# Kernel tuning notes

Hardware: AMD Instinct MI355X
Metric: run time of the kernel (lower is better)

Reference implementation:

```python
import jax, jax.numpy as jnp
import numpy as np

N = 100000
INC = 128
GRID = 256
S = 2  # scale s for voxel_to_aux coarse pooling


def _ln(x, g, b, eps=1e-6):
    m = jnp.mean(x, axis=-1, keepdims=True)
    v = jnp.var(x, axis=-1, keepdims=True)
    return (x - m) / jnp.sqrt(v + eps) * g + b


def setup_inputs() -> dict:
    rng = np.random.default_rng(0)
    lin = rng.choice(GRID ** 3, size=N, replace=False)
    x = (lin // (GRID * GRID)).astype(np.int64)
    y = ((lin // GRID) % GRID).astype(np.int64)
    z = (lin % GRID).astype(np.int64)
    coords = np.stack([x, y, z], axis=1).astype(np.int32)
    # sparse 3x3x3 neighbor table (pad index = N for missing neighbors)
    order = np.argsort(lin)
    lin_sorted = lin[order]
    nbr_idx = np.full((N, 27), N, dtype=np.int32)
    k = 0
    for dx in (-1, 0, 1):
        for dy in (-1, 0, 1):
            for dz in (-1, 0, 1):
                nx, ny, nz = x + dx, y + dy, z + dz
                valid = (nx >= 0) & (nx < GRID) & (ny >= 0) & (ny < GRID) & (nz >= 0) & (nz < GRID)
                nlin = (nx * GRID + ny) * GRID + nz
                pos = np.clip(np.searchsorted(lin_sorted, nlin), 0, N - 1)
                found = valid & (lin_sorted[pos] == nlin)
                nbr_idx[:, k] = np.where(found, order[pos].astype(np.int32), N)
                k += 1
    # voxel_to_aux: coarse voxel id at scale S; counts per coarse voxel
    G2 = GRID // S
    clin = ((x // S) * G2 + (y // S)) * G2 + (z // S)
    uniq, aux_idx, counts = np.unique(clin, return_inverse=True, return_counts=True)
    counts_v = counts[aux_idx].astype(np.float32)
    num_aux = int(len(uniq))

    key = jax.random.key(0)
    ks = jax.random.split(key, 6)
    sd = 1.0 / np.sqrt(INC)
    return {
        "F": jax.random.normal(ks[0], (N, INC), jnp.float32),
        "coords": jnp.asarray(coords),
        "nbr_idx": jnp.asarray(nbr_idx),
        "aux_idx": jnp.asarray(aux_idx.astype(np.int32)),
        "counts_v": jnp.asarray(counts_v),
        "num_aux": num_aux,
        "alpha": jnp.ones((1, INC), jnp.float32),
        "w_pos": jax.random.normal(ks[1], (INC, 3), jnp.float32) * (1.0 / np.sqrt(3.0)),
        "w_pre": jax.random.normal(ks[2], (INC, INC), jnp.float32) * sd,
        "g_pre": jnp.ones((INC,), jnp.float32),
        "b_pre": jnp.zeros((INC,), jnp.float32),
        "w_conv": jax.random.normal(ks[3], (27, INC, INC), jnp.float32) * (sd / np.sqrt(27.0)),
        "g_local": jnp.ones((INC,), jnp.float32),
        "b_local": jnp.zeros((INC,), jnp.float32),
        "g_norm": jnp.ones((INC,), jnp.float32),
        "b_norm": jnp.zeros((INC,), jnp.float32),
    }


def reference(F, coords, nbr_idx, aux_idx, counts_v, num_aux, alpha, w_pos, w_pre,
              g_pre, b_pre, w_conv, g_local, b_local, g_norm, b_norm):
    inc = F.shape[1]
    # pre_mix: Linear (no bias) + LayerNorm
    F_input = _ln(F @ w_pre.T, g_pre, b_pre)
    # local_mix: sparse 3x3x3 conv on ORIGINAL features via neighbor gather
    Fp = jnp.concatenate([F, jnp.zeros((1, inc), F.dtype)], axis=0)
    gathered = Fp[nbr_idx]                               # [N, 27, inc]
    local = jnp.einsum('nkc,kcd->nd', gathered, w_conv)  # [N, inc]
    # cos_x positional reweighting
    pos = (coords.astype(jnp.float32) @ w_pos.T) * alpha  # [N, inc]
    psin, pcos = jnp.sin(pos), jnp.cos(pos)
    cat = jnp.concatenate([F_input * pcos, F_input * psin, F_input * pos], axis=1)  # [N, 3*inc]
    # voxel_to_aux (sum pool per coarse voxel) + aux_to_voxel (mean broadcast back)
    aux = jax.ops.segment_sum(cat, aux_idx, num_segments=num_aux)
    vox = aux[aux_idx] / counts_v[:, None]
    new = (vox[:, :inc] * pcos + vox[:, inc:2 * inc] * psin
           + (vox[:, 2 * inc:] - F_input * pos))
    new = _ln(new, g_norm, b_norm)
    local = _ln(local, g_local, b_local)
    return jax.nn.relu(new + local)
```

## Files before the change

kernel.cpp:

```cpp
#include <hip/hip_runtime.h>
#include <hip/hip_bf16.h>
#include <stdint.h>

#define N_PTS 100000
#define INC 128
#define NSLOT 27
#define CAPP 8192
#define SCAP 64

typedef float f32x4 __attribute__((ext_vector_type(4)));
typedef short bf16x8 __attribute__((ext_vector_type(8)));

static const size_t OFF_WP   = 0;
static const size_t SZ_WP    = (size_t)NSLOT * INC * INC * 2;
static const size_t OFF_WPRE = (OFF_WP + SZ_WP + 255) & ~(size_t)255;
static const size_t SZ_WPRE  = (size_t)INC * INC * 2;
static const size_t OFF_FIN  = (OFF_WPRE + SZ_WPRE + 255) & ~(size_t)255;
static const size_t SZ_FIN   = (size_t)N_PTS * INC * 2;
static const size_t OFF_LOC  = (OFF_FIN + SZ_FIN + 255) & ~(size_t)255;
static const size_t SZ_LOC   = (size_t)N_PTS * INC * 4;
static const size_t OFF_LOC2 = (OFF_LOC + SZ_LOC + 255) & ~(size_t)255;
static const size_t SZ_LOC2  = (size_t)N_PTS * INC * 4;
static const size_t OFF_CNT  = (OFF_LOC2 + SZ_LOC2 + 255) & ~(size_t)255;
static const size_t SZ_CNT   = 128;
static const size_t OFF_DST  = (OFF_CNT + SZ_CNT + 255) & ~(size_t)255;
static const size_t SZ_DST   = (size_t)26 * CAPP * 4;
static const size_t OFF_SRC  = (OFF_DST + SZ_DST + 255) & ~(size_t)255;
static const size_t SZ_SRC   = (size_t)26 * CAPP * 4;
static const size_t OFF_FLG  = (OFF_SRC + SZ_SRC + 255) & ~(size_t)255;
static const size_t SZ_FLG   = (size_t)N_PTS;
static const size_t OFF_NDL  = (OFF_FLG + SZ_FLG + 255) & ~(size_t)255;
static const size_t SZ_NDL   = (size_t)N_PTS * 4;

#define PREP_BLOCKS 1792
#define SCAN_BLOCKS 391
#define MT64 1563
#define PAIRB 256

__device__ __forceinline__ float compute_pos3(float w0, float w1, float w2, float a,
                                              float cx, float cy, float cz) {
    return (cx * w0 + cy * w1 + cz * w2) * a;
}

__device__ __forceinline__ bf16x8 ld_cvt8(const float* __restrict__ p) {
    const float4 u = *(const float4*)p;
    const float4 v = *(const float4*)(p + 4);
    bf16x8 r;
    __hip_bfloat16* h = (__hip_bfloat16*)&r;
    h[0] = __float2bfloat16(u.x); h[1] = __float2bfloat16(u.y);
    h[2] = __float2bfloat16(u.z); h[3] = __float2bfloat16(u.w);
    h[4] = __float2bfloat16(v.x); h[5] = __float2bfloat16(v.y);
    h[6] = __float2bfloat16(v.z); h[7] = __float2bfloat16(v.w);
    return r;
}

__global__ __launch_bounds__(256) void k_front(
        const float* __restrict__ w_pre, const float* __restrict__ w_conv,
        __hip_bfloat16* __restrict__ Wp, __hip_bfloat16* __restrict__ Wpre,
        const int* __restrict__ nbr_idx, const float* __restrict__ counts_v,
        int* __restrict__ cnt, int* __restrict__ dst, int* __restrict__ src,
        unsigned char* __restrict__ flg, int* __restrict__ ndl,
        float* __restrict__ loc2) {
    __shared__ int s_cnt[26], s_base[26];
    __shared__ int s_dst[26][SCAP], s_src[26][SCAP];

    const int tid = threadIdx.x;

    if (blockIdx.x < PREP_BLOCKS) {
        int i = blockIdx.x * 256 + tid;
        if (i < 16384) {
            int d = i >> 7, c = i & 127;
            int j = ((c >> 5) << 12) | ((d >> 4) << 9)
                  | (((((c >> 3) & 3) << 4) + (d & 15)) << 3) | (c & 7);
            Wpre[j] = __float2bfloat16(w_pre[i]);
        } else if (i < 16384 + NSLOT * 16384) {
            int t = i - 16384;
            int slot = t >> 14, rem = t & 16383;
            int c = rem >> 7, d = rem & 127;
            int j = (slot << 14) | ((c >> 5) << 12) | ((d >> 4) << 9)
                  | (((((c >> 3) & 3) << 4) + (d & 15)) << 3) | (c & 7);
            Wp[j] = __float2bfloat16(w_conv[t]);
        }
        return;
    }

    const int lane = tid & 63;
    const int p = (blockIdx.x - PREP_BLOCKS) * 256 + tid;
    const bool vp = p < N_PTS;

    if (tid < 26) s_cnt[tid] = 0;
    __syncthreads();

    float cv = vp ? counts_v[p] : 0.f;
    bool multi = cv > 1.5f;

    const int* nb = nbr_idx + (size_t)p * NSLOT;
    bool hn = false;
#pragma unroll 1
    for (int k = 0; k < NSLOT; ++k) {
        if (k == 13) continue;
        int m = vp ? nb[k] : N_PTS;
        if (m < N_PTS) {
            hn = true;
            int b = k < 13 ? k : k - 1;
            int li = atomicAdd(&s_cnt[b], 1);
            if (li < SCAP) { s_dst[b][li] = p; s_src[b][li] = m; }
            else {
                int gi = atomicAdd(&cnt[b], 1);
                if (gi < CAPP) { dst[b * CAPP + gi] = p; src[b * CAPP + gi] = m; }
            }
        }
    }

    bool nd = vp && (hn || multi);
    if (vp) flg[p] = (unsigned char)(nd ? 1 : 0);
    if (nd) {
        float4* row = (float4*)(loc2 + (size_t)p * INC);
#pragma unroll
        for (int i = 0; i < INC / 4; ++i) row[i] = make_float4(0.f, 0.f, 0.f, 0.f);
    }
    unsigned long long mb = __ballot(nd);
    int basew = 0;
    if (lane == 0 && mb) basew = atomicAdd(&cnt[26], __popcll(mb));
    basew = __shfl(basew, 0);
    if (nd) ndl[basew + __popcll(mb & ((1ull << lane) - 1))] = p;

    __syncthreads();

    if (tid < 26) {
        int n = s_cnt[tid]; if (n > SCAP) n = SCAP;
        s_base[tid] = n > 0 ? atomicAdd(&cnt[tid], n) : 0;
        s_cnt[tid] = n;
    }
    __syncthreads();

    for (int b = tid >> 3; b < 26; b += 32) {
        int n = s_cnt[b], base = s_base[b];
        for (int e = tid & 7; e < n; e += 8) {
            int gi = base + e;
            if (gi < CAPP) { dst[b * CAPP + gi] = s_dst[b][e]; src[b * CAPP + gi] = s_src[b][e]; }
        }
    }
}

__global__ __launch_bounds__(256, 3) void k_main(
        const float* __restrict__ F, const __hip_bfloat16* __restrict__ Wpre,
        const __hip_bfloat16* __restrict__ Wp, const unsigned char* __restrict__ flg,
        const float* __restrict__ g_pre, const float* __restrict__ b_pre,
        const float* __restrict__ g_local, const float* __restrict__ b_local,
        const float* __restrict__ g_norm, const float* __restrict__ b_norm,
        const int* __restrict__ cnt, const int* __restrict__ dst,
        const int* __restrict__ src,
        __hip_bfloat16* __restrict__ F_input, float* __restrict__ loc,
        float* __restrict__ loc2, float* __restrict__ outp) {
    __shared__ __hip_bfloat16 s_bf[4][16 * 136];
    __shared__ float s_gp[INC], s_bp[INC], s_gl[INC], s_bl[INC], s_gn[INC], s_bn[INC];
    __shared__ int s_wre[27], s_cntb[26];

    const int tid = threadIdx.x, w = tid >> 6, lane = tid & 63;
    const int q = lane >> 4, l15 = lane & 15;

    if (blockIdx.x >= MT64) {
        const int pb = blockIdx.x - MT64;
        if (tid == 0) {
            int accw = 0; s_wre[0] = 0;
            for (int b = 0; b < 26; ++b) {
                int v = cnt[b]; if (v > CAPP) v = CAPP;
                s_cntb[b] = v;
                accw += (v + 15) >> 4;
                s_wre[b + 1] = accw;
            }
        }
        __syncthreads();
        const int W = s_wre[26];
#pragma unroll 1
        for (int wvi = pb * 4 + w; wvi < W; wvi += PAIRB * 4) {
            int b = 0;
            while (wvi >= s_wre[b + 1]) ++b;
            int base = (wvi - s_wre[b]) << 4;
            int nB = s_cntb[b];
            int slot = b < 13 ? b : b + 1;
            const int* srcb = src + b * CAPP;
            const int* dstb = dst + b * CAPP;
            int mrow = (base + l15 < nB) ? srcb[base + l15] : 0;
            const bf16x8* Bp = (const bf16x8*)Wp + (size_t)slot * 2048;

            f32x4 acc[8];
#pragma unroll
            for (int j = 0; j < 8; ++j) acc[j] = (f32x4){0.f, 0.f, 0.f, 0.f};
#pragma unroll
            for (int ks = 0; ks < 4; ++ks) {
                bf16x8 a2 = ld_cvt8(F + (size_t)mrow * INC + ks * 32 + q * 8);
#pragma unroll
                for (int j = 0; j < 8; ++j)
                    acc[j] = __builtin_amdgcn_mfma_f32_16x16x32_bf16(
                        a2, Bp[(ks * 8 + j) * 64 + lane], acc[j], 0, 0, 0);
            }
#pragma unroll
            for (int r = 0; r < 4; ++r) {
                int m = (q << 2) + r;
                int ri = base + m;
                if (ri < nB) {
                    int d = dstb[ri];
                    float* lp = loc2 + (size_t)d * INC + l15;
#pragma unroll
                    for (int j = 0; j < 8; ++j) atomicAdd(lp + (j << 4), acc[j][r]);
                }
            }
        }
        return;
    }

    const int p0 = blockIdx.x * 64;

    if (tid < INC) {
        s_gp[tid] = g_pre[tid];   s_bp[tid] = b_pre[tid];
        s_gl[tid] = g_local[tid]; s_bl[tid] = b_local[tid];
        s_gn[tid] = g_norm[tid];  s_bn[tid] = b_norm[tid];
    }
    __syncthreads();

    int grow = p0 + (w << 4) + l15;
    if (grow >= N_PTS) grow = N_PTS - 1;

    const float* A = F + (size_t)grow * INC + q * 8;

    unsigned int fe = *(const unsigned int*)(flg + p0 + (w << 4) + (q << 2));
    unsigned char fs0 = flg[p0 + (w << 4) + q];
    unsigned char fs1 = flg[p0 + (w << 4) + 4 + q];
    unsigned char fs2 = flg[p0 + (w << 4) + 8 + q];
    unsigned char fs3 = flg[p0 + (w << 4) + 12 + q];

    bf16x8 a[4];
#pragma unroll
    for (int ks = 0; ks < 4; ++ks) a[ks] = ld_cvt8(A + ks * 32);

    const bf16x8* BP = (const bf16x8*)Wpre;
    const bf16x8* BL = (const bf16x8*)Wp + (size_t)13 * 2048;
    f32x4 accP[8], accL[8];
#pragma unroll
    for (int j = 0; j < 8; ++j) {
        accP[j] = (f32x4){0.f, 0.f, 0.f, 0.f};
        accL[j] = (f32x4){0.f, 0.f, 0.f, 0.f};
    }
    bf16x8 bP[8], bL[8];
#pragma unroll
    for (int j = 0; j < 8; ++j) bP[j] = BP[j * 64 + lane];
#pragma unroll
    for (int ks = 0; ks < 4; ++ks) {
#pragma unroll
        for (int j = 0; j < 8; ++j) bL[j] = BL[(ks * 8 + j) * 64 + lane];
#pragma unroll
        for (int j = 0; j < 8; ++j)
            accP[j] = __builtin_amdgcn_mfma_f32_16x16x32_bf16(a[ks], bP[j], accP[j], 0, 0, 0);
        if (ks < 3) {
#pragma unroll
            for (int j = 0; j < 8; ++j) bP[j] = BP[((ks + 1) * 8 + j) * 64 + lane];
        }
#pragma unroll
        for (int j = 0; j < 8; ++j)
            accL[j] = __builtin_amdgcn_mfma_f32_16x16x32_bf16(a[ks], bL[j], accL[j], 0, 0, 0);
    }

    __hip_bfloat16* sb = s_bf[w];
#pragma unroll
    for (int r = 0; r < 4; ++r) {
        int ri = (q << 2) + r;
        int p = p0 + (w << 4) + ri;
        int fl = (p < N_PTS) ? (int)((fe >> (r * 8)) & 1) : 1;

        float s = 0.f, ss = 0.f;
#pragma unroll
        for (int j = 0; j < 8; ++j) { float v = accP[j][r]; s += v; ss += v * v; }
#pragma unroll
        for (int m = 1; m < 16; m <<= 1) { s += __shfl_xor(s, m); ss += __shfl_xor(ss, m); }
        float mean = s * (1.f / 128.f);
        float rstd = rsqrtf(ss * (1.f / 128.f) - mean * mean + 1e-6f);

        float fj[8], sN = 0.f, ssN = 0.f, sL = 0.f, ssL = 0.f;
#pragma unroll
        for (int j = 0; j < 8; ++j) {
            int c = (j << 4) + l15;
            float fi = (accP[j][r] - mean) * rstd * s_gp[c] + s_bp[c];
            __hip_bfloat16 fb = __float2bfloat16(fi);
            sb[ri * 136 + c] = fb;
            float f = __bfloat162float(fb);
            fj[j] = f; sN += f; ssN += f * f;
            float v = accL[j][r]; sL += v; ssL += v * v;
        }
#pragma unroll
        for (int m = 1; m < 16; m <<= 1) {
            sN += __shfl_xor(sN, m); ssN += __shfl_xor(ssN, m);
            sL += __shfl_xor(sL, m); ssL += __shfl_xor(ssL, m);
        }
        float meanN = sN * (1.f / 128.f);
        float rstdN = rsqrtf(ssN * (1.f / 128.f) - meanN * meanN + 1e-6f);
        float meanL = sL * (1.f / 128.f);
        float rstdL = rsqrtf(ssL * (1.f / 128.f) - meanL * meanL + 1e-6f);

        if (p < N_PTS) {
            float* dp = fl ? (loc + (size_t)p * INC) : (outp + (size_t)p * INC);
#pragma unroll
            for (int j = 0; j < 8; ++j) {
                int c = (j << 4) + l15;
                float lvj = accL[j][r];
                float nn = (fj[j] - meanN) * rstdN * s_gn[c] + s_bn[c];
                float ll = (lvj - meanL) * rstdL * s_gl[c] + s_bl[c];
                float o = nn + ll; o = o > 0.f ? o : 0.f;
                dp[c] = fl ? lvj : o;
            }
        }
    }

    {
        unsigned char fsv[4] = {fs0, fs1, fs2, fs3};
#pragma unroll
        for (int t = 0; t < 4; ++t) {
            int row = (t << 2) + q;
            int p = p0 + (w << 4) + row;
            if (p < N_PTS && (fsv[t] & 1)) {
                bf16x8 v = *(const bf16x8*)&sb[row * 136 + l15 * 8];
                *(bf16x8*)(F_input + (size_t)p * INC + l15 * 8) = v;
            }
        }
    }
}

__global__ __launch_bounds__(256) void k_final(
        const __hip_bfloat16* __restrict__ F_input, const float* __restrict__ loc,
        const float* __restrict__ loc2,
        const int* __restrict__ nbr_idx, const int* __restrict__ coords,
        const float* __restrict__ counts_v,
        const float* __restrict__ w_pos, const float* __restrict__ alpha,
        const float* __restrict__ g_local, const float* __restrict__ b_local,
        const float* __restrict__ g_norm, const float* __restrict__ b_norm,
        const int* __restrict__ cnt, const int* __restrict__ ndl,
        float* __restrict__ out) {
    const int tid = threadIdx.x, g = tid >> 4, l15 = tid & 15;
    const int c0 = l15 * 8;
    const int nd = cnt[26];
    if (blockIdx.x * 64 >= nd) return;

    float wpv[24], pa[8], gl[8], bl[8], gn[8], bn[8];
#pragma unroll
    for (int t = 0; t < 6; ++t) ((float4*)wpv)[t] = ((const float4*)(w_pos + c0 * 3))[t];
#pragma unroll
    for (int t = 0; t < 2; ++t) {
        ((float4*)pa)[t] = ((const float4*)(alpha   + c0))[t];
        ((float4*)gl)[t] = ((const float4*)(g_local + c0))[t];
        ((float4*)bl)[t] = ((const float4*)(b_local + c0))[t];
        ((float4*)gn)[t] = ((const float4*)(g_norm  + c0))[t];
        ((float4*)bn)[t] = ((const float4*)(b_norm  + c0))[t];
    }

    for (int base = blockIdx.x * 64; base < nd; base += gridDim.x * 64) {
#pragma unroll 1
        for (int t = 0; t < 4; ++t) {
            int idx = base + t * 16 + g;
            if (idx >= nd) continue;
            int p = ndl[idx];

            float lv[8], s = 0.f, ss = 0.f;
            float4 la0 = *(const float4*)(loc  + (size_t)p * INC + c0);
            float4 la1 = *(const float4*)(loc  + (size_t)p * INC + c0 + 4);
            float4 lb0 = *(const float4*)(loc2 + (size_t)p * INC + c0);
            float4 lb1 = *(const float4*)(loc2 + (size_t)p * INC + c0 + 4);
            lv[0] = la0.x + lb0.x; lv[1] = la0.y + lb0.y;
            lv[2] = la0.z + lb0.z; lv[3] = la0.w + lb0.w;
            lv[4] = la1.x + lb1.x; lv[5] = la1.y + lb1.y;
            lv[6] = la1.z + lb1.z; lv[7] = la1.w + lb1.w;
#pragma unroll
            for (int j = 0; j < 8; ++j) { s += lv[j]; ss += lv[j] * lv[j]; }
#pragma unroll
            for (int m = 1; m < 16; m <<= 1) { s += __shfl_xor(s, m); ss += __shfl_xor(ss, m); }
            float meanL = s * (1.f / 128.f);
            float rstdL = rsqrtf(ss * (1.f / 128.f) - meanL * meanL + 1e-6f);

            float cv = counts_v[p];
            bool multi = cv > 1.5f;
            int ix = coords[p * 3 + 0], iy = coords[p * 3 + 1], iz = coords[p * 3 + 2];
            float cx = (float)ix, cy = (float)iy, cz = (float)iz;

            bf16x8 fbv = *(const bf16x8*)(F_input + (size_t)p * INC + c0);

            float psO[8], snO[8], csO[8], fO[8];
#pragma unroll
            for (int j = 0; j < 8; ++j) {
                fO[j] = __bfloat162float(((__hip_bfloat16*)&fbv)[j]);
                psO[j] = compute_pos3(wpv[j * 3], wpv[j * 3 + 1], wpv[j * 3 + 2], pa[j], cx, cy, cz);
                snO[j] = __sinf(psO[j]); csO[j] = __cosf(psO[j]);
            }

            float v0[8], v1[8], v2[8];
            if (multi) {
                float invc = 1.f / cv;
                int ox = (ix & 1) ? -1 : 1, oy = (iy & 1) ? -1 : 1, oz = (iz & 1) ? -1 : 1;
                const int* nb = nbr_idx + (size_t)p * NSLOT;
                float wt8[8], mx8[8], my8[8], mz8[8];
                bf16x8 fmv8[8];
#pragma unroll
                for (int e = 0; e < 8; ++e) {
                    int dx = (e & 4) ? ox : 0, dy = (e & 2) ? oy : 0, dz = (e & 1) ? oz : 0;
                    int m = (e == 0) ? p : nb[(dx + 1) * 9 + (dy + 1) * 3 + (dz + 1)];
                    bool ok = m < N_PTS;
                    wt8[e] = ok ? 1.f : 0.f;
                    int mc = ok ? m : p;
                    fmv8[e] = *(const bf16x8*)(F_input + (size_t)mc * INC + c0);
                    mx8[e] = cx + (float)dx; my8[e] = cy + (float)dy; mz8[e] = cz + (float)dz;
                }
#pragma unroll
                for (int j = 0; j < 8; ++j) { v0[j] = 0.f; v1[j] = 0.f; v2[j] = 0.f; }
#pragma unroll
                for (int e = 0; e < 8; ++e) {
#pragma unroll
                    for (int j = 0; j < 8; ++j) {
                        float fm = wt8[e] * __bfloat162float(((__hip_bfloat16*)&fmv8[e])[j]);
                        float ps = compute_pos3(wpv[j * 3], wpv[j * 3 + 1], wpv[j * 3 + 2], pa[j],
                                                mx8[e], my8[e], mz8[e]);
                        v0[j] += fm * __cosf(ps);
                        v1[j] += fm * __sinf(ps);
                        v2[j] += fm * ps;
                    }
                }
#pragma unroll
                for (int j = 0; j < 8; ++j) { v0[j] *= invc; v1[j] *= invc; v2[j] *= invc; }
            } else {
#pragma unroll
                for (int j = 0; j < 8; ++j) {
                    v0[j] = fO[j] * csO[j]; v1[j] = fO[j] * snO[j]; v2[j] = fO[j] * psO[j];
                }
            }

            float nv[8], s2 = 0.f, ss2 = 0.f;
#pragma unroll
            for (int j = 0; j < 8; ++j) {
                float nw = v0[j] * csO[j] + v1[j] * snO[j] + v2[j] - fO[j] * psO[j];
                nv[j] = nw; s2 += nw; ss2 += nw * nw;
            }
#pragma unroll
            for (int m = 1; m < 16; m <<= 1) { s2 += __shfl_xor(s2, m); ss2 += __shfl_xor(ss2, m); }
            float meanN = s2 * (1.f / 128.f);
            float rstdN = rsqrtf(ss2 * (1.f / 128.f) - meanN * meanN + 1e-6f);
            float ov[8];
#pragma unroll
            for (int j = 0; j < 8; ++j) {
                float nn = (nv[j] - meanN) * rstdN * gn[j] + bn[j];
                float ll = (lv[j] - meanL) * rstdL * gl[j] + bl[j];
                float o = nn + ll;
                ov[j] = o > 0.f ? o : 0.f;
            }
            float4* op = (float4*)(out + (size_t)p * INC + c0);
            op[0] = ((float4*)ov)[0];
            op[1] = ((float4*)ov)[1];
        }
    }
}

extern "C" void kernel_launch(void* const* d_in, const int* in_sizes, int n_in,
                              void* d_out, int out_size, void* d_ws, size_t ws_size,
                              hipStream_t stream) {
    (void)in_sizes; (void)n_in; (void)out_size; (void)ws_size;
    const float* F        = (const float*)d_in[0];
    const int*   coords   = (const int*)d_in[1];
    const int*   nbr      = (const int*)d_in[2];
    const float* counts_v = (const float*)d_in[4];
    const float* alpha    = (const float*)d_in[6];
    const float* w_pos    = (const float*)d_in[7];
    const float* w_pre    = (const float*)d_in[8];
    const float* g_pre    = (const float*)d_in[9];
    const float* b_pre    = (const float*)d_in[10];
    const float* w_conv   = (const float*)d_in[11];
    const float* g_local  = (const float*)d_in[12];
    const float* b_local  = (const float*)d_in[13];
    const float* g_norm   = (const float*)d_in[14];
    const float* b_norm   = (const float*)d_in[15];
    float* out = (float*)d_out;

    char* ws = (char*)d_ws;
    __hip_bfloat16* Wp      = (__hip_bfloat16*)(ws + OFF_WP);
    __hip_bfloat16* Wpre    = (__hip_bfloat16*)(ws + OFF_WPRE);
    __hip_bfloat16* F_input = (__hip_bfloat16*)(ws + OFF_FIN);
    float*          loc     = (float*)(ws + OFF_LOC);
    float*          loc2    = (float*)(ws + OFF_LOC2);
    int*            cnt     = (int*)(ws + OFF_CNT);
    int*            dstb    = (int*)(ws + OFF_DST);
    int*            srcb    = (int*)(ws + OFF_SRC);
    unsigned char*  flg     = (unsigned char*)(ws + OFF_FLG);
    int*            ndl     = (int*)(ws + OFF_NDL);

    hipMemsetAsync(cnt, 0, SZ_CNT, stream);
    k_front<<<PREP_BLOCKS + SCAN_BLOCKS, 256, 0, stream>>>(
        w_pre, w_conv, Wp, Wpre, nbr, counts_v, cnt, dstb, srcb, flg, ndl, loc2);
    k_main<<<MT64 + PAIRB, 256, 0, stream>>>(
        F, Wpre, Wp, flg, g_pre, b_pre, g_local, b_local, g_norm, b_norm,
        cnt, dstb, srcb, F_input, loc, loc2, out);
    k_final<<<512, 256, 0, stream>>>(F_input, loc, loc2, nbr, coords, counts_v,
                                     w_pos, alpha, g_local, b_local, g_norm, b_norm,
                                     cnt, ndl, out);
}
```

Before: 219.0 us.

## Replace shared-memory neighbor bucketing with wave-level ballot atomics and retile final kernel

The neighbor-pair bucketing in k_front now uses per-wave ballot plus one global atomic per slot instead of shared-memory staging with block barriers, and neighbor indices are preloaded into registers with the loop fully unrolled. k_main reads the bucket counts in parallel before the serial prefix. k_final processes 16 points per block-iteration instead of 64, drops the inner t-loop, and launches twice as many blocks. The aim is fewer barriers and less shared-memory traffic, plus better load balance in the final pass. The cost is more global atomics and less coalesced dst/src writes.

```diff
diff --git a/kernel.cpp b/kernel.cpp
--- a/kernel.cpp
+++ b/kernel.cpp
@@ -6,7 +6,6 @@
 #define INC 128
 #define NSLOT 27
 #define CAPP 8192
-#define SCAP 64
 
 typedef float f32x4 __attribute__((ext_vector_type(4)));
 typedef short bf16x8 __attribute__((ext_vector_type(8)));
@@ -61,9 +60,6 @@
         int* __restrict__ cnt, int* __restrict__ dst, int* __restrict__ src,
         unsigned char* __restrict__ flg, int* __restrict__ ndl,
         float* __restrict__ loc2) {
-    __shared__ int s_cnt[26], s_base[26];
-    __shared__ int s_dst[26][SCAP], s_src[26][SCAP];
-
     const int tid = threadIdx.x;
 
     if (blockIdx.x < PREP_BLOCKS) {
@@ -88,59 +84,46 @@
     const int p = (blockIdx.x - PREP_BLOCKS) * 256 + tid;
     const bool vp = p < N_PTS;
 
-    if (tid < 26) s_cnt[tid] = 0;
-    __syncthreads();
-
     float cv = vp ? counts_v[p] : 0.f;
     bool multi = cv > 1.5f;
 
     const int* nb = nbr_idx + (size_t)p * NSLOT;
+    int nbr_r[NSLOT];
+#pragma unroll
+    for (int k = 0; k < NSLOT; ++k) nbr_r[k] = vp ? nb[k] : N_PTS;
+
     bool hn = false;
-#pragma unroll 1
+#pragma unroll
     for (int k = 0; k < NSLOT; ++k) {
         if (k == 13) continue;
-        int m = vp ? nb[k] : N_PTS;
-        if (m < N_PTS) {
-            hn = true;
+        int m = nbr_r[k];
+        bool valid = (m < N_PTS);
+        hn = hn || valid;
+        unsigned long long msk = __ballot(valid);
+        if (msk) {
             int b = k < 13 ? k : k - 1;
-            int li = atomicAdd(&s_cnt[b], 1);
-            if (li < SCAP) { s_dst[b][li] = p; s_src[b][li] = m; }
-            else {
-                int gi = atomicAdd(&cnt[b], 1);
+            int basew = 0;
+            if (lane == 0) basew = atomicAdd(&cnt[b], __popcll(msk));
+            basew = __shfl(basew, 0);
+            if (valid) {
+                int gi = basew + __popcll(msk & ((1ull << lane) - 1ull));
                 if (gi < CAPP) { dst[b * CAPP + gi] = p; src[b * CAPP + gi] = m; }
             }
         }
     }
 
-    bool nd = vp && (hn || multi);
-    if (vp) flg[p] = (unsigned char)(nd ? 1 : 0);
-    if (nd) {
+    bool ndv = vp && (hn || multi);
+    if (vp) flg[p] = (unsigned char)(ndv ? 1 : 0);
+    if (ndv) {
         float4* row = (float4*)(loc2 + (size_t)p * INC);
 #pragma unroll
         for (int i = 0; i < INC / 4; ++i) row[i] = make_float4(0.f, 0.f, 0.f, 0.f);
     }
-    unsigned long long mb = __ballot(nd);
-    int basew = 0;
-    if (lane == 0 && mb) basew = atomicAdd(&cnt[26], __popcll(mb));
-    basew = __shfl(basew, 0);
-    if (nd) ndl[basew + __popcll(mb & ((1ull << lane) - 1))] = p;
-
-    __syncthreads();
-
-    if (tid < 26) {
-        int n = s_cnt[tid]; if (n > SCAP) n = SCAP;
-        s_base[tid] = n > 0 ? atomicAdd(&cnt[tid], n) : 0;
-        s_cnt[tid] = n;
-    }
-    __syncthreads();
-
-    for (int b = tid >> 3; b < 26; b += 32) {
-        int n = s_cnt[b], base = s_base[b];
-        for (int e = tid & 7; e < n; e += 8) {
-            int gi = base + e;
-            if (gi < CAPP) { dst[b * CAPP + gi] = s_dst[b][e]; src[b * CAPP + gi] = s_src[b][e]; }
-        }
-    }
+    unsigned long long mb = __ballot(ndv);
+    int basew2 = 0;
+    if (lane == 0 && mb) basew2 = atomicAdd(&cnt[26], __popcll(mb));
+    basew2 = __shfl(basew2, 0);
+    if (ndv) ndl[basew2 + __popcll(mb & ((1ull << lane) - 1ull))] = p;
 }
 
 __global__ __launch_bounds__(256, 3) void k_main(
@@ -162,14 +145,11 @@
 
     if (blockIdx.x >= MT64) {
         const int pb = blockIdx.x - MT64;
+        if (tid < 26) { int v = cnt[tid]; if (v > CAPP) v = CAPP; s_cntb[tid] = v; }
+        __syncthreads();
         if (tid == 0) {
             int accw = 0; s_wre[0] = 0;
-            for (int b = 0; b < 26; ++b) {
-                int v = cnt[b]; if (v > CAPP) v = CAPP;
-                s_cntb[b] = v;
-                accw += (v + 15) >> 4;
-                s_wre[b + 1] = accw;
-            }
+            for (int b = 0; b < 26; ++b) { accw += (s_cntb[b] + 15) >> 4; s_wre[b + 1] = accw; }
         }
         __syncthreads();
         const int W = s_wre[26];
@@ -339,7 +319,7 @@
     const int tid = threadIdx.x, g = tid >> 4, l15 = tid & 15;
     const int c0 = l15 * 8;
     const int nd = cnt[26];
-    if (blockIdx.x * 64 >= nd) return;
+    if (blockIdx.x * 16 >= nd) return;
 
     float wpv[24], pa[8], gl[8], bl[8], gn[8], bn[8];
 #pragma unroll
@@ -353,106 +333,106 @@
         ((float4*)bn)[t] = ((const float4*)(b_norm  + c0))[t];
     }
 
-    for (int base = blockIdx.x * 64; base < nd; base += gridDim.x * 64) {
-#pragma unroll 1
-        for (int t = 0; t < 4; ++t) {
-            int idx = base + t * 16 + g;
-            if (idx >= nd) continue;
-            int p = ndl[idx];
-
-            float lv[8], s = 0.f, ss = 0.f;
-            float4 la0 = *(const float4*)(loc  + (size_t)p * INC + c0);
-            float4 la1 = *(const float4*)(loc  + (size_t)p * INC + c0 + 4);
-            float4 lb0 = *(const float4*)(loc2 + (size_t)p * INC + c0);
-            float4 lb1 = *(const float4*)(loc2 + (size_t)p * INC + c0 + 4);
-            lv[0] = la0.x + lb0.x; lv[1] = la0.y + lb0.y;
-            lv[2] = la0.z + lb0.z; lv[3] = la0.w + lb0.w;
-            lv[4] = la1.x + lb1.x; lv[5] = la1.y + lb1.y;
-            lv[6] = la1.z + lb1.z; lv[7] = la1.w + lb1.w;
-#pragma unroll
-            for (int j = 0; j < 8; ++j) { s += lv[j]; ss += lv[j] * lv[j]; }
-#pragma unroll
-            for (int m = 1; m < 16; m <<= 1) { s += __shfl_xor(s, m); ss += __shfl_xor(ss, m); }
-            float meanL = s * (1.f / 128.f);
-            float rstdL = rsqrtf(ss * (1.f / 128.f) - meanL * meanL + 1e-6f);
-
-            float cv = counts_v[p];
-            bool multi = cv > 1.5f;
-            int ix = coords[p * 3 + 0], iy = coords[p * 3 + 1], iz = coords[p * 3 + 2];
-            float cx = (float)ix, cy = (float)iy, cz = (float)iz;
-
-            bf16x8 fbv = *(const bf16x8*)(F_input + (size_t)p * INC + c0);
-
-            float psO[8], snO[8], csO[8], fO[8];
+    for (int base = blockIdx.x * 16; base < nd; base += gridDim.x * 16) {
+        int idx = base + g;
+        if (idx >= nd) continue;
+        int p = ndl[idx];
+
+        float lv[8], s = 0.f, ss = 0.f;
+        float4 la0 = *(const float4*)(loc  + (size_t)p * INC + c0);
+        float4 la1 = *(const float4*)(loc  + (size_t)p * INC + c0 + 4);
+        float4 lb0 = *(const float4*)(loc2 + (size_t)p * INC + c0);
+        float4 lb1 = *(const float4*)(loc2 + (size_t)p * INC + c0 + 4);
+        lv[0] = la0.x + lb0.x; lv[1] = la0.y + lb0.y;
+        lv[2] = la0.z + lb0.z; lv[3] = la0.w + lb0.w;
+        lv[4] = la1.x + lb1.x; lv[5] = la1.y + lb1.y;
+        lv[6] = la1.z + lb1.z; lv[7] = la1.w + lb1.w;
+#pragma unroll
+        for (int j = 0; j < 8; ++j) { s += lv[j]; ss += lv[j] * lv[j]; }
+#pragma unroll
+        for (int m = 1; m < 16; m <<= 1) { s += __shfl_xor(s, m); ss += __shfl_xor(ss, m); }
+        float meanL = s * (1.f / 128.f);
+        float rstdL = rsqrtf(ss * (1.f / 128.f) - meanL * meanL + 1e-6f);
+
+        float cv = counts_v[p];
+        bool multi = cv > 1.5f;
+        int ix = coords[p * 3 + 0], iy = coords[p * 3 + 1], iz = coords[p * 3 + 2];
+        float cx = (float)ix, cy = (float)iy, cz = (float)iz;
+
+        bf16x8 fbv = *(const bf16x8*)(F_input + (size_t)p * INC + c0);
+
+        float psO[8], snO[8], csO[8], fO[8];
+#pragma unroll
+        for (int j = 0; j < 8; ++j) {
+            fO[j] = __bfloat162float(((__hip_bfloat16*)&fbv)[j]);
+            psO[j] = compute_pos3(wpv[j * 3], wpv[j * 3 + 1], wpv[j * 3 + 2], pa[j], cx, cy, cz);
+            snO[j] = __sinf(psO[j]); csO[j] = __cosf(psO[j]);
+        }
+
+        float v0[8], v1[8], v2[8];
+        if (multi) {
+            float invc = 1.f / cv;
+            int ox = (ix & 1) ? -1 : 1, oy = (iy & 1) ? -1 : 1, oz = (iz & 1) ? -1 : 1;
+            const int* nb = nbr_idx + (size_t)p * NSLOT;
+            unsigned vmask = 1u;
+            bf16x8 fmv8[8];
+            fmv8[0] = fbv;
+#pragma unroll
+            for (int e = 1; e < 8; ++e) {
+                int dx = (e & 4) ? ox : 0, dy = (e & 2) ? oy : 0, dz = (e & 1) ? oz : 0;
+                int m = nb[(dx + 1) * 9 + (dy + 1) * 3 + (dz + 1)];
+                bool ok = m < N_PTS;
+                if (ok) vmask |= (1u << e);
+                int mc = ok ? m : p;
+                fmv8[e] = *(const bf16x8*)(F_input + (size_t)mc * INC + c0);
+            }
+#pragma unroll
+            for (int j = 0; j < 8; ++j) { v0[j] = 0.f; v1[j] = 0.f; v2[j] = 0.f; }
+#pragma unroll
+            for (int e = 0; e < 8; ++e) {
+                float wt = ((vmask >> e) & 1u) ? 1.f : 0.f;
+                int dx = (e & 4) ? ox : 0, dy = (e & 2) ? oy : 0, dz = (e & 1) ? oz : 0;
+                float mx = cx + (float)dx, my = cy + (float)dy, mz = cz + (float)dz;
+#pragma unroll
+                for (int j = 0; j < 8; ++j) {
+                    float fm = wt * __bfloat162float(((__hip_bfloat16*)&fmv8[e])[j]);
+                    float ps = compute_pos3(wpv[j * 3], wpv[j * 3 + 1], wpv[j * 3 + 2], pa[j],
+                                            mx, my, mz);
+                    v0[j] += fm * __cosf(ps);
+                    v1[j] += fm * __sinf(ps);
+                    v2[j] += fm * ps;
+                }
+            }
+#pragma unroll
+            for (int j = 0; j < 8; ++j) { v0[j] *= invc; v1[j] *= invc; v2[j] *= invc; }
+        } else {
 #pragma unroll
             for (int j = 0; j < 8; ++j) {
-                fO[j] = __bfloat162float(((__hip_bfloat16*)&fbv)[j]);
-                psO[j] = compute_pos3(wpv[j * 3], wpv[j * 3 + 1], wpv[j * 3 + 2], pa[j], cx, cy, cz);
-                snO[j] = __sinf(psO[j]); csO[j] = __cosf(psO[j]);
-            }
-
-            float v0[8], v1[8], v2[8];
-            if (multi) {
-                float invc = 1.f / cv;
-                int ox = (ix & 1) ? -1 : 1, oy = (iy & 1) ? -1 : 1, oz = (iz & 1) ? -1 : 1;
-                const int* nb = nbr_idx + (size_t)p * NSLOT;
-                float wt8[8], mx8[8], my8[8], mz8[8];
-                bf16x8 fmv8[8];
-#pragma unroll
-                for (int e = 0; e < 8; ++e) {
-                    int dx = (e & 4) ? ox : 0, dy = (e & 2) ? oy : 0, dz = (e & 1) ? oz : 0;
-                    int m = (e == 0) ? p : nb[(dx + 1) * 9 + (dy + 1) * 3 + (dz + 1)];
-                    bool ok = m < N_PTS;
-                    wt8[e] = ok ? 1.f : 0.f;
-                    int mc = ok ? m : p;
-                    fmv8[e] = *(const bf16x8*)(F_input + (size_t)mc * INC + c0);
-                    mx8[e] = cx + (float)dx; my8[e] = cy + (float)dy; mz8[e] = cz + (float)dz;
-                }
-#pragma unroll
-                for (int j = 0; j < 8; ++j) { v0[j] = 0.f; v1[j] = 0.f; v2[j] = 0.f; }
-#pragma unroll
-                for (int e = 0; e < 8; ++e) {
-#pragma unroll
-                    for (int j = 0; j < 8; ++j) {
-                        float fm = wt8[e] * __bfloat162float(((__hip_bfloat16*)&fmv8[e])[j]);
-                        float ps = compute_pos3(wpv[j * 3], wpv[j * 3 + 1], wpv[j * 3 + 2], pa[j],
-                                                mx8[e], my8[e], mz8[e]);
-                        v0[j] += fm * __cosf(ps);
-                        v1[j] += fm * __sinf(ps);
-                        v2[j] += fm * ps;
-                    }
-                }
-#pragma unroll
-                for (int j = 0; j < 8; ++j) { v0[j] *= invc; v1[j] *= invc; v2[j] *= invc; }
-            } else {
-#pragma unroll
-                for (int j = 0; j < 8; ++j) {
-                    v0[j] = fO[j] * csO[j]; v1[j] = fO[j] * snO[j]; v2[j] = fO[j] * psO[j];
-                }
-            }
-
-            float nv[8], s2 = 0.f, ss2 = 0.f;
-#pragma unroll
-            for (int j = 0; j < 8; ++j) {
-                float nw = v0[j] * csO[j] + v1[j] * snO[j] + v2[j] - fO[j] * psO[j];
-                nv[j] = nw; s2 += nw; ss2 += nw * nw;
-            }
-#pragma unroll
-            for (int m = 1; m < 16; m <<= 1) { s2 += __shfl_xor(s2, m); ss2 += __shfl_xor(ss2, m); }
-            float meanN = s2 * (1.f / 128.f);
-            float rstdN = rsqrtf(ss2 * (1.f / 128.f) - meanN * meanN + 1e-6f);
-            float ov[8];
-#pragma unroll
-            for (int j = 0; j < 8; ++j) {
-                float nn = (nv[j] - meanN) * rstdN * gn[j] + bn[j];
-                float ll = (lv[j] - meanL) * rstdL * gl[j] + bl[j];
-                float o = nn + ll;
-                ov[j] = o > 0.f ? o : 0.f;
-            }
-            float4* op = (float4*)(out + (size_t)p * INC + c0);
-            op[0] = ((float4*)ov)[0];
-            op[1] = ((float4*)ov)[1];
-        }
+                v0[j] = fO[j] * csO[j]; v1[j] = fO[j] * snO[j]; v2[j] = fO[j] * psO[j];
+            }
+        }
+
+        float nv[8], s2 = 0.f, ss2 = 0.f;
+#pragma unroll
+        for (int j = 0; j < 8; ++j) {
+            float nw = v0[j] * csO[j] + v1[j] * snO[j] + v2[j] - fO[j] * psO[j];
+            nv[j] = nw; s2 += nw; ss2 += nw * nw;
+        }
+#pragma unroll
+        for (int m = 1; m < 16; m <<= 1) { s2 += __shfl_xor(s2, m); ss2 += __shfl_xor(ss2, m); }
+        float meanN = s2 * (1.f / 128.f);
+        float rstdN = rsqrtf(ss2 * (1.f / 128.f) - meanN * meanN + 1e-6f);
+        float ov[8];
+#pragma unroll
+        for (int j = 0; j < 8; ++j) {
+            float nn = (nv[j] - meanN) * rstdN * gn[j] + bn[j];
+            float ll = (lv[j] - meanL) * rstdL * gl[j] + bl[j];
+            float o = nn + ll;
+            ov[j] = o > 0.f ? o : 0.f;
+        }
+        float4* op = (float4*)(out + (size_t)p * INC + c0);
+        op[0] = ((float4*)ov)[0];
+        op[1] = ((float4*)ov)[1];
     }
 }
 
@@ -494,7 +474,7 @@
     k_main<<<MT64 + PAIRB, 256, 0, stream>>>(
         F, Wpre, Wp, flg, g_pre, b_pre, g_local, b_local, g_norm, b_norm,
         cnt, dstb, srcb, F_input, loc, loc2, out);
-    k_final<<<512, 256, 0, stream>>>(F_input, loc, loc2, nbr, coords, counts_v,
-                                     w_pos, alpha, g_local, b_local, g_norm, b_norm,
-                                     cnt, ndl, out);
-}
+    k_final<<<1024, 256, 0, stream>>>(F_input, loc, loc2, nbr, coords, counts_v,
+                                      w_pos, alpha, g_local, b_local, g_norm, b_norm,
+                                      cnt, ndl, out);
+}
```

Result: slower. 317.2 us (+44.8%).
